# Performance work log

Measured on AMD Instinct MI355X. Metric: run time of the kernel, lower is better.

Reference implementation:

```python
import jax, jax.numpy as jnp
import numpy as np

B, H, O, M = 8192, 1024, 1024, 4

def setup_inputs() -> dict:
    key = jax.random.key(0)
    ks = jax.random.split(key, 8)
    state = jax.random.normal(ks[0], (B, H), dtype=jnp.float32)
    spectral_entropy = jax.random.uniform(ks[1], (B, 1), dtype=jnp.float32)
    curvature = jax.random.normal(ks[2], (B, 1), dtype=jnp.float32)
    # learned params
    modulation_basis = jax.random.normal(ks[3], (M, H, O), dtype=jnp.float32)
    gate_w = jax.random.normal(ks[4], (1, M), dtype=jnp.float32) / jnp.sqrt(1.0)
    gate_b = jax.random.normal(ks[5], (M,), dtype=jnp.float32) * 0.01
    prj_w = jax.random.normal(ks[6], (H, O), dtype=jnp.float32) / jnp.sqrt(H)
    prj_b = jax.random.normal(ks[7], (O,), dtype=jnp.float32) * 0.01
    return {"state": state, "spectral_entropy": spectral_entropy, "curvature": curvature,
            "modulation_basis": modulation_basis, "gate_w": gate_w, "gate_b": gate_b,
            "prj_w": prj_w, "prj_b": prj_b}

def reference(state, spectral_entropy, curvature, modulation_basis, gate_w, gate_b, prj_w, prj_b):
    # softmax gate over modes: [B, M]
    mod_weights = jax.nn.softmax(spectral_entropy @ gate_w + gate_b, axis=-1)
    # Algebraically fused form of einsum('bm,mho->bho') then einsum('bh,bho->bo'):
    # compute per-mode matvec results [B, M, O] (small), then mode-weighted sum.
    mode_out = jnp.einsum('bh,mho->bmo', state, modulation_basis)
    mischief_output = jnp.einsum('bm,bmo->bo', mod_weights, mode_out)
    base_output = state @ prj_w + prj_b
    mix = jax.nn.sigmoid(curvature)  # [B, 1]
    return (1.0 - mix) * base_output + mix * mischief_output
```

## Files before the change

### kernel.cpp

```cpp
#include <hip/hip_runtime.h>
#include <stdint.h>

typedef __attribute__((ext_vector_type(4))) float  float4v;
typedef __attribute__((ext_vector_type(8))) __bf16 bf16x8;
typedef __attribute__((ext_vector_type(8))) unsigned short ushort8;

#define B_DIM 8192
#define H_DIM 1024
#define O_DIM 1024

static __device__ __forceinline__ unsigned short f32_to_bf16(float f) {
  union { float f; unsigned int u; } v; v.f = f;
  unsigned int u = v.u;
  unsigned int r = u + 0x7FFFu + ((u >> 16) & 1u);
  return (unsigned short)(r >> 16);
}

__global__ void prep_coeff(const float* __restrict__ se, const float* __restrict__ curv,
                           const float* __restrict__ gw, const float* __restrict__ gb,
                           float* __restrict__ cfg) {
  int b = blockIdx.x * blockDim.x + threadIdx.x;
  if (b >= B_DIM) return;
  float s = se[b];
  float l0 = s * gw[0] + gb[0];
  float l1 = s * gw[1] + gb[1];
  float l2 = s * gw[2] + gb[2];
  float l3 = s * gw[3] + gb[3];
  float mx = fmaxf(fmaxf(l0, l1), fmaxf(l2, l3));
  float e0 = __expf(l0 - mx), e1 = __expf(l1 - mx), e2 = __expf(l2 - mx), e3 = __expf(l3 - mx);
  float mix = 1.0f / (1.0f + __expf(-curv[b]));
  float inv = mix / (e0 + e1 + e2 + e3);
  cfg[0 * B_DIM + b] = e0 * inv;
  cfg[1 * B_DIM + b] = e1 * inv;
  cfg[2 * B_DIM + b] = e2 * inv;
  cfg[3 * B_DIM + b] = e3 * inv;
  cfg[4 * B_DIM + b] = 1.0f - mix;
}

__global__ void cast_state(const float* __restrict__ src, unsigned short* __restrict__ dst, int n8) {
  int i = blockIdx.x * blockDim.x + threadIdx.x;
  if (i >= n8) return;
  float4v v0 = ((const float4v*)src)[i * 2];
  float4v v1 = ((const float4v*)src)[i * 2 + 1];
  ushort8 o;
  o[0] = f32_to_bf16(v0.x); o[1] = f32_to_bf16(v0.y);
  o[2] = f32_to_bf16(v0.z); o[3] = f32_to_bf16(v0.w);
  o[4] = f32_to_bf16(v1.x); o[5] = f32_to_bf16(v1.y);
  o[6] = f32_to_bf16(v1.z); o[7] = f32_to_bf16(v1.w);
  ((ushort8*)dst)[i] = o;
}

__global__ void transpose_cast(const float* __restrict__ basis, const float* __restrict__ prjw,
                               unsigned short* __restrict__ Wt) {
  __shared__ __align__(16) unsigned short t[64 * 72];
  int m = blockIdx.z;
  const float* src = (m < 4) ? (basis + (size_t)m * H_DIM * O_DIM) : prjw;
  int o0 = blockIdx.x * 64, h0 = blockIdx.y * 64;
  int tid = threadIdx.x;
  int r  = tid >> 4;
  int c4 = (tid & 15) * 4;
#pragma unroll
  for (int p = 0; p < 4; ++p) {
    int h = r + p * 16;
    float4v v = *(const float4v*)(src + (size_t)(h0 + h) * O_DIM + o0 + c4);
    t[(c4 + 0) * 72 + h] = f32_to_bf16(v.x);
    t[(c4 + 1) * 72 + h] = f32_to_bf16(v.y);
    t[(c4 + 2) * 72 + h] = f32_to_bf16(v.z);
    t[(c4 + 3) * 72 + h] = f32_to_bf16(v.w);
  }
  __syncthreads();
#pragma unroll
  for (int i = 0; i < 2; ++i) {
    int C = i * 256 + tid;
    int o = C >> 3, cc = C & 7;
    ushort8 val = *(const ushort8*)(t + o * 72 + cc * 8);
    *(ushort8*)(Wt + ((size_t)m * O_DIM + o0 + o) * H_DIM + h0 + cc * 8) = val;
  }
}

__global__ __launch_bounds__(256, 2)
void gemm_fused(const unsigned short* __restrict__ A,
                const unsigned short* __restrict__ Wt,
                const float* __restrict__ cfg,
                const float* __restrict__ prjb,
                float* __restrict__ out) {
  __shared__ __align__(16) unsigned char smem[59904];
  unsigned short* sA  = (unsigned short*)smem;
  unsigned short* sB  = (unsigned short*)(smem + 16384);
  float*          scf = (float*)(smem + 57344);

  const int tid  = threadIdx.x;
  const int lane = tid & 63;
  const int wave = tid >> 6;
  const int row0 = blockIdx.x * 128;
  const int col0 = blockIdx.y * 64;
  const int wrow = (wave >> 1) * 64;
  const int wcol = (wave & 1) * 32;
  const int q  = lane >> 4;
  const int ln = lane & 15;

  for (int i = tid; i < 5 * 128; i += 256)
    scf[i] = cfg[(i >> 7) * B_DIM + row0 + (i & 127)];

  int arow[4], acol[4];
#pragma unroll
  for (int j = 0; j < 4; ++j) {
    int L = (wave * 4 + j) * 64 + lane;
    arow[j] = L >> 3;
    acol[j] = (L & 7) ^ (arow[j] & 7);
  }
  int brow[2], bcol[2];
#pragma unroll
  for (int j = 0; j < 2; ++j) {
    int L = (wave * 2 + j) * 64 + lane;
    brow[j] = L >> 3;
    bcol[j] = (L & 7) ^ (brow[j] & 7);
  }

  float4v acc[5][4][2];
#pragma unroll
  for (int m = 0; m < 5; ++m)
#pragma unroll
    for (int i = 0; i < 4; ++i)
#pragma unroll
      for (int j = 0; j < 2; ++j)
        acc[m][i][j] = (float4v){0.f, 0.f, 0.f, 0.f};

  for (int kt = 0; kt < 16; ++kt) {
    const int k0 = kt * 64;
    __syncthreads();
#pragma unroll
    for (int j = 0; j < 4; ++j) {
      const unsigned short* ga = A + (size_t)(row0 + arow[j]) * H_DIM + k0 + acol[j] * 8;
      unsigned short* la = sA + (wave * 4 + j) * 512;
      __builtin_amdgcn_global_load_lds(
          (const __attribute__((address_space(1))) void*)ga,
          (__attribute__((address_space(3))) void*)la, 16, 0, 0);
    }
#pragma unroll
    for (int m = 0; m < 5; ++m) {
      const unsigned short* Wm = Wt + (size_t)m * O_DIM * H_DIM;
#pragma unroll
      for (int j = 0; j < 2; ++j) {
        const unsigned short* gw = Wm + (size_t)(col0 + brow[j]) * H_DIM + k0 + bcol[j] * 8;
        unsigned short* lb = sB + m * 4096 + (wave * 2 + j) * 512;
        __builtin_amdgcn_global_load_lds(
            (const __attribute__((address_space(1))) void*)gw,
            (__attribute__((address_space(3))) void*)lb, 16, 0, 0);
      }
    }
    __syncthreads();

#pragma unroll
    for (int kk = 0; kk < 2; ++kk) {
      bf16x8 af[4];
#pragma unroll
      for (int t = 0; t < 4; ++t) {
        int ra = wrow + t * 16 + ln;
        int ca = (kk * 4 + q) ^ (ra & 7);
        af[t] = *(const bf16x8*)(sA + ra * 64 + ca * 8);
      }
#pragma unroll
      for (int m = 0; m < 5; ++m) {
        bf16x8 b0, b1;
        {
          int rb = wcol + ln;
          int cb = (kk * 4 + q) ^ (rb & 7);
          b0 = *(const bf16x8*)(sB + m * 4096 + rb * 64 + cb * 8);
          int rb1 = wcol + 16 + ln;
          int cb1 = (kk * 4 + q) ^ (rb1 & 7);
          b1 = *(const bf16x8*)(sB + m * 4096 + rb1 * 64 + cb1 * 8);
        }
#pragma unroll
        for (int ti = 0; ti < 4; ++ti) {
          acc[m][ti][0] = __builtin_amdgcn_mfma_f32_16x16x32_bf16(af[ti], b0, acc[m][ti][0], 0, 0, 0);
          acc[m][ti][1] = __builtin_amdgcn_mfma_f32_16x16x32_bf16(af[ti], b1, acc[m][ti][1], 0, 0, 0);
        }
      }
    }
  }

  __syncthreads();
  float* fbuf = (float*)smem;
#pragma unroll
  for (int ti = 0; ti < 4; ++ti) {
    int rl = wrow + ti * 16 + q * 4;
#pragma unroll
    for (int tj = 0; tj < 2; ++tj) {
      int cc = wcol + tj * 16 + ln;
#pragma unroll
      for (int r = 0; r < 4; ++r) {
        float v = 0.f;
#pragma unroll
        for (int m = 0; m < 5; ++m)
          v += scf[m * 128 + rl + r] * acc[m][ti][tj][r];
        fbuf[(rl + r) * 68 + cc] = v;
      }
    }
  }
  __syncthreads();
#pragma unroll
  for (int i = 0; i < 8; ++i) {
    int L = i * 256 + tid;
    int row = L >> 4, c4 = L & 15;
    float4v v = *(const float4v*)(fbuf + row * 68 + c4 * 4);
    float cb = scf[4 * 128 + row];
    float4v pb = *(const float4v*)(prjb + col0 + c4 * 4);
    v += cb * pb;
    *(float4v*)(out + (size_t)(row0 + row) * O_DIM + col0 + c4 * 4) = v;
  }
}

extern "C" void kernel_launch(void* const* d_in, const int* in_sizes, int n_in,
                              void* d_out, int out_size, void* d_ws, size_t ws_size,
                              hipStream_t stream) {
  const float* state = (const float*)d_in[0];
  const float* se    = (const float*)d_in[1];
  const float* curv  = (const float*)d_in[2];
  const float* basis = (const float*)d_in[3];
  const float* gw    = (const float*)d_in[4];
  const float* gb    = (const float*)d_in[5];
  const float* prjw  = (const float*)d_in[6];
  const float* prjb  = (const float*)d_in[7];
  float* out = (float*)d_out;

  char* ws = (char*)d_ws;
  unsigned short* Abf = (unsigned short*)ws;
  unsigned short* Wt  = (unsigned short*)(ws + (size_t)16 * 1024 * 1024);
  float* cfg          = (float*)(ws + (size_t)28 * 1024 * 1024);

  prep_coeff<<<B_DIM / 256, 256, 0, stream>>>(se, curv, gw, gb, cfg);
  cast_state<<<(B_DIM * H_DIM / 8) / 256, 256, 0, stream>>>(state, Abf, B_DIM * H_DIM / 8);
  dim3 tg(O_DIM / 64, H_DIM / 64, 5);
  transpose_cast<<<tg, 256, 0, stream>>>(basis, prjw, Wt);
  dim3 gg(B_DIM / 128, O_DIM / 64);
  gemm_fused<<<gg, 256, 0, stream>>>(Abf, Wt, cfg, prjb, out);
}
```

Before: 184.0 us.

## Double-buffer GEMM K-loop with smaller K tile and merge prep kernels

The main GEMM now uses a two-stage LDS double buffer with a K tile of 32 instead of a single-buffered K tile of 64. The next stage's global-to-LDS loads are issued before computing the current stage, and there is one barrier per stage. The gate/softmax coefficients are computed inside the GEMM rather than in a separate kernel, and the state cast and weight transpose-cast are merged into one launch. The goal is to overlap memory loads with MFMA work and cut launch count, at the cost of a new swizzle scheme, more loop iterations and a shallower K tile per barrier.

```diff
diff --git a/kernel.cpp b/kernel.cpp
--- a/kernel.cpp
+++ b/kernel.cpp
@@ -16,78 +16,59 @@
   return (unsigned short)(r >> 16);
 }
 
-__global__ void prep_coeff(const float* __restrict__ se, const float* __restrict__ curv,
-                           const float* __restrict__ gw, const float* __restrict__ gb,
-                           float* __restrict__ cfg) {
-  int b = blockIdx.x * blockDim.x + threadIdx.x;
-  if (b >= B_DIM) return;
-  float s = se[b];
-  float l0 = s * gw[0] + gb[0];
-  float l1 = s * gw[1] + gb[1];
-  float l2 = s * gw[2] + gb[2];
-  float l3 = s * gw[3] + gb[3];
-  float mx = fmaxf(fmaxf(l0, l1), fmaxf(l2, l3));
-  float e0 = __expf(l0 - mx), e1 = __expf(l1 - mx), e2 = __expf(l2 - mx), e3 = __expf(l3 - mx);
-  float mix = 1.0f / (1.0f + __expf(-curv[b]));
-  float inv = mix / (e0 + e1 + e2 + e3);
-  cfg[0 * B_DIM + b] = e0 * inv;
-  cfg[1 * B_DIM + b] = e1 * inv;
-  cfg[2 * B_DIM + b] = e2 * inv;
-  cfg[3 * B_DIM + b] = e3 * inv;
-  cfg[4 * B_DIM + b] = 1.0f - mix;
-}
-
-__global__ void cast_state(const float* __restrict__ src, unsigned short* __restrict__ dst, int n8) {
-  int i = blockIdx.x * blockDim.x + threadIdx.x;
-  if (i >= n8) return;
-  float4v v0 = ((const float4v*)src)[i * 2];
-  float4v v1 = ((const float4v*)src)[i * 2 + 1];
-  ushort8 o;
-  o[0] = f32_to_bf16(v0.x); o[1] = f32_to_bf16(v0.y);
-  o[2] = f32_to_bf16(v0.z); o[3] = f32_to_bf16(v0.w);
-  o[4] = f32_to_bf16(v1.x); o[5] = f32_to_bf16(v1.y);
-  o[6] = f32_to_bf16(v1.z); o[7] = f32_to_bf16(v1.w);
-  ((ushort8*)dst)[i] = o;
-}
-
-__global__ void transpose_cast(const float* __restrict__ basis, const float* __restrict__ prjw,
-                               unsigned short* __restrict__ Wt) {
+__global__ void prep_inputs(const float* __restrict__ state,
+                            const float* __restrict__ basis,
+                            const float* __restrict__ prjw,
+                            unsigned short* __restrict__ Abf,
+                            unsigned short* __restrict__ Wt) {
   __shared__ __align__(16) unsigned short t[64 * 72];
-  int m = blockIdx.z;
-  const float* src = (m < 4) ? (basis + (size_t)m * H_DIM * O_DIM) : prjw;
-  int o0 = blockIdx.x * 64, h0 = blockIdx.y * 64;
+  int bb = blockIdx.x;
   int tid = threadIdx.x;
-  int r  = tid >> 4;
-  int c4 = (tid & 15) * 4;
-#pragma unroll
-  for (int p = 0; p < 4; ++p) {
-    int h = r + p * 16;
-    float4v v = *(const float4v*)(src + (size_t)(h0 + h) * O_DIM + o0 + c4);
-    t[(c4 + 0) * 72 + h] = f32_to_bf16(v.x);
-    t[(c4 + 1) * 72 + h] = f32_to_bf16(v.y);
-    t[(c4 + 2) * 72 + h] = f32_to_bf16(v.z);
-    t[(c4 + 3) * 72 + h] = f32_to_bf16(v.w);
-  }
-  __syncthreads();
-#pragma unroll
-  for (int i = 0; i < 2; ++i) {
-    int C = i * 256 + tid;
-    int o = C >> 3, cc = C & 7;
-    ushort8 val = *(const ushort8*)(t + o * 72 + cc * 8);
-    *(ushort8*)(Wt + ((size_t)m * O_DIM + o0 + o) * H_DIM + h0 + cc * 8) = val;
+  if (bb < 1280) {
+    int m = bb >> 8, panel = bb & 255;
+    int o0 = (panel & 15) * 64, h0 = (panel >> 4) * 64;
+    const float* src = (m < 4) ? (basis + (size_t)m * H_DIM * O_DIM) : prjw;
+    int r  = tid >> 4;
+    int c4 = (tid & 15) * 4;
+#pragma unroll
+    for (int p = 0; p < 4; ++p) {
+      int h = r + p * 16;
+      float4v v = *(const float4v*)(src + (size_t)(h0 + h) * O_DIM + o0 + c4);
+      t[(c4 + 0) * 72 + h] = f32_to_bf16(v.x);
+      t[(c4 + 1) * 72 + h] = f32_to_bf16(v.y);
+      t[(c4 + 2) * 72 + h] = f32_to_bf16(v.z);
+      t[(c4 + 3) * 72 + h] = f32_to_bf16(v.w);
+    }
+    __syncthreads();
+#pragma unroll
+    for (int i = 0; i < 2; ++i) {
+      int C = i * 256 + tid;
+      int o = C >> 3, cc = C & 7;
+      ushort8 val = *(const ushort8*)(t + o * 72 + cc * 8);
+      *(ushort8*)(Wt + ((size_t)m * O_DIM + o0 + o) * H_DIM + h0 + cc * 8) = val;
+    }
+  } else {
+    int i = (bb - 1280) * 256 + tid;
+    float4v v0 = ((const float4v*)state)[i * 2];
+    float4v v1 = ((const float4v*)state)[i * 2 + 1];
+    ushort8 o;
+    o[0] = f32_to_bf16(v0.x); o[1] = f32_to_bf16(v0.y);
+    o[2] = f32_to_bf16(v0.z); o[3] = f32_to_bf16(v0.w);
+    o[4] = f32_to_bf16(v1.x); o[5] = f32_to_bf16(v1.y);
+    o[6] = f32_to_bf16(v1.z); o[7] = f32_to_bf16(v1.w);
+    ((ushort8*)Abf)[i] = o;
   }
 }
 
 __global__ __launch_bounds__(256, 2)
 void gemm_fused(const unsigned short* __restrict__ A,
                 const unsigned short* __restrict__ Wt,
-                const float* __restrict__ cfg,
+                const float* __restrict__ se, const float* __restrict__ curv,
+                const float* __restrict__ gw, const float* __restrict__ gb,
                 const float* __restrict__ prjb,
                 float* __restrict__ out) {
   __shared__ __align__(16) unsigned char smem[59904];
-  unsigned short* sA  = (unsigned short*)smem;
-  unsigned short* sB  = (unsigned short*)(smem + 16384);
-  float*          scf = (float*)(smem + 57344);
+  float* scf = (float*)(smem + 57344);
 
   const int tid  = threadIdx.x;
   const int lane = tid & 63;
@@ -99,22 +80,44 @@
   const int q  = lane >> 4;
   const int ln = lane & 15;
 
-  for (int i = tid; i < 5 * 128; i += 256)
-    scf[i] = cfg[(i >> 7) * B_DIM + row0 + (i & 127)];
-
-  int arow[4], acol[4];
-#pragma unroll
-  for (int j = 0; j < 4; ++j) {
-    int L = (wave * 4 + j) * 64 + lane;
-    arow[j] = L >> 3;
-    acol[j] = (L & 7) ^ (arow[j] & 7);
-  }
-  int brow[2], bcol[2];
+  if (tid < 128) {
+    int b = row0 + tid;
+    float s = se[b];
+    float l0 = fmaf(s, gw[0], gb[0]);
+    float l1 = fmaf(s, gw[1], gb[1]);
+    float l2 = fmaf(s, gw[2], gb[2]);
+    float l3 = fmaf(s, gw[3], gb[3]);
+    float mx = fmaxf(fmaxf(l0, l1), fmaxf(l2, l3));
+    float e0 = __expf(l0 - mx), e1 = __expf(l1 - mx);
+    float e2 = __expf(l2 - mx), e3 = __expf(l3 - mx);
+    float mix = 1.0f / (1.0f + __expf(-curv[b]));
+    float inv = mix / (e0 + e1 + e2 + e3);
+    scf[0 * 128 + tid] = e0 * inv;
+    scf[1 * 128 + tid] = e1 * inv;
+    scf[2 * 128 + tid] = e2 * inv;
+    scf[3 * 128 + tid] = e3 * inv;
+    scf[4 * 128 + tid] = 1.0f - mix;
+  }
+
+  const unsigned short* gA[2];
+  unsigned int ldsA[2];
 #pragma unroll
   for (int j = 0; j < 2; ++j) {
-    int L = (wave * 2 + j) * 64 + lane;
-    brow[j] = L >> 3;
-    bcol[j] = (L & 7) ^ (brow[j] & 7);
+    int C = (wave * 2 + j) * 64 + lane;
+    int row = C >> 2, pos = C & 3;
+    int g = pos ^ ((row >> 1) & 3);
+    gA[j] = A + (size_t)(row0 + row) * H_DIM + g * 8;
+    ldsA[j] = (wave * 2 + j) * 1024;
+  }
+  const unsigned short* gB[5];
+  unsigned int ldsBbase = 8192 + wave * 1024;
+  {
+    int C = wave * 64 + lane;
+    int row = C >> 2, pos = C & 3;
+    int g = pos ^ ((row >> 1) & 3);
+#pragma unroll
+    for (int m = 0; m < 5; ++m)
+      gB[m] = Wt + (size_t)m * O_DIM * H_DIM + (size_t)(col0 + row) * H_DIM + g * 8;
   }
 
   float4v acc[5][4][2];
@@ -126,59 +129,65 @@
       for (int j = 0; j < 2; ++j)
         acc[m][i][j] = (float4v){0.f, 0.f, 0.f, 0.f};
 
-  for (int kt = 0; kt < 16; ++kt) {
-    const int k0 = kt * 64;
+#define ISSUE_STAGE(s)                                                          \
+  do {                                                                          \
+    const int _buf = (s) & 1;                                                   \
+    const int _k = (s) * 32;                                                    \
+    unsigned char* _base = smem + _buf * 28672;                                 \
+    _Pragma("unroll")                                                           \
+    for (int _j = 0; _j < 2; ++_j)                                              \
+      __builtin_amdgcn_global_load_lds(                                         \
+          (const __attribute__((address_space(1))) void*)(gA[_j] + _k),         \
+          (__attribute__((address_space(3))) void*)(_base + ldsA[_j]), 16, 0, 0);\
+    _Pragma("unroll")                                                           \
+    for (int _m = 0; _m < 5; ++_m)                                              \
+      __builtin_amdgcn_global_load_lds(                                         \
+          (const __attribute__((address_space(1))) void*)(gB[_m] + _k),         \
+          (__attribute__((address_space(3))) void*)(_base + ldsBbase + _m * 4096),\
+          16, 0, 0);                                                            \
+  } while (0)
+
+#define COMPUTE_STAGE(s)                                                        \
+  do {                                                                          \
+    const unsigned short* _sA = (const unsigned short*)(smem + ((s) & 1) * 28672);\
+    const unsigned short* _sB = _sA + 4096;                                     \
+    bf16x8 _af[4];                                                              \
+    _Pragma("unroll")                                                           \
+    for (int _t = 0; _t < 4; ++_t) {                                            \
+      int _ra = wrow + _t * 16 + ln;                                            \
+      int _ps = q ^ ((_ra >> 1) & 3);                                           \
+      _af[_t] = *(const bf16x8*)(_sA + _ra * 32 + _ps * 8);                     \
+    }                                                                           \
+    _Pragma("unroll")                                                           \
+    for (int _m = 0; _m < 5; ++_m) {                                            \
+      bf16x8 _b0, _b1;                                                          \
+      {                                                                         \
+        int _rb = wcol + ln;                                                    \
+        int _p0 = q ^ ((_rb >> 1) & 3);                                         \
+        _b0 = *(const bf16x8*)(_sB + _m * 2048 + _rb * 32 + _p0 * 8);           \
+        int _r1 = wcol + 16 + ln;                                               \
+        int _p1 = q ^ ((_r1 >> 1) & 3);                                         \
+        _b1 = *(const bf16x8*)(_sB + _m * 2048 + _r1 * 32 + _p1 * 8);           \
+      }                                                                         \
+      _Pragma("unroll")                                                         \
+      for (int _ti = 0; _ti < 4; ++_ti) {                                       \
+        acc[_m][_ti][0] = __builtin_amdgcn_mfma_f32_16x16x32_bf16(              \
+            _af[_ti], _b0, acc[_m][_ti][0], 0, 0, 0);                           \
+        acc[_m][_ti][1] = __builtin_amdgcn_mfma_f32_16x16x32_bf16(              \
+            _af[_ti], _b1, acc[_m][_ti][1], 0, 0, 0);                           \
+      }                                                                         \
+    }                                                                           \
+  } while (0)
+
+  ISSUE_STAGE(0);
+  __syncthreads();
+#pragma unroll 2
+  for (int s = 0; s < 31; ++s) {
+    ISSUE_STAGE(s + 1);
+    COMPUTE_STAGE(s);
     __syncthreads();
-#pragma unroll
-    for (int j = 0; j < 4; ++j) {
-      const unsigned short* ga = A + (size_t)(row0 + arow[j]) * H_DIM + k0 + acol[j] * 8;
-      unsigned short* la = sA + (wave * 4 + j) * 512;
-      __builtin_amdgcn_global_load_lds(
-          (const __attribute__((address_space(1))) void*)ga,
-          (__attribute__((address_space(3))) void*)la, 16, 0, 0);
-    }
-#pragma unroll
-    for (int m = 0; m < 5; ++m) {
-      const unsigned short* Wm = Wt + (size_t)m * O_DIM * H_DIM;
-#pragma unroll
-      for (int j = 0; j < 2; ++j) {
-        const unsigned short* gw = Wm + (size_t)(col0 + brow[j]) * H_DIM + k0 + bcol[j] * 8;
-        unsigned short* lb = sB + m * 4096 + (wave * 2 + j) * 512;
-        __builtin_amdgcn_global_load_lds(
-            (const __attribute__((address_space(1))) void*)gw,
-            (__attribute__((address_space(3))) void*)lb, 16, 0, 0);
-      }
-    }
-    __syncthreads();
-
-#pragma unroll
-    for (int kk = 0; kk < 2; ++kk) {
-      bf16x8 af[4];
-#pragma unroll
-      for (int t = 0; t < 4; ++t) {
-        int ra = wrow + t * 16 + ln;
-        int ca = (kk * 4 + q) ^ (ra & 7);
-        af[t] = *(const bf16x8*)(sA + ra * 64 + ca * 8);
-      }
-#pragma unroll
-      for (int m = 0; m < 5; ++m) {
-        bf16x8 b0, b1;
-        {
-          int rb = wcol + ln;
-          int cb = (kk * 4 + q) ^ (rb & 7);
-          b0 = *(const bf16x8*)(sB + m * 4096 + rb * 64 + cb * 8);
-          int rb1 = wcol + 16 + ln;
-          int cb1 = (kk * 4 + q) ^ (rb1 & 7);
-          b1 = *(const bf16x8*)(sB + m * 4096 + rb1 * 64 + cb1 * 8);
-        }
-#pragma unroll
-        for (int ti = 0; ti < 4; ++ti) {
-          acc[m][ti][0] = __builtin_amdgcn_mfma_f32_16x16x32_bf16(af[ti], b0, acc[m][ti][0], 0, 0, 0);
-          acc[m][ti][1] = __builtin_amdgcn_mfma_f32_16x16x32_bf16(af[ti], b1, acc[m][ti][1], 0, 0, 0);
-        }
-      }
-    }
-  }
+  }
+  COMPUTE_STAGE(31);
 
   __syncthreads();
   float* fbuf = (float*)smem;
@@ -209,6 +218,8 @@
     v += cb * pb;
     *(float4v*)(out + (size_t)(row0 + row) * O_DIM + col0 + c4 * 4) = v;
   }
+#undef ISSUE_STAGE
+#undef COMPUTE_STAGE
 }
 
 extern "C" void kernel_launch(void* const* d_in, const int* in_sizes, int n_in,
@@ -227,12 +238,8 @@
   char* ws = (char*)d_ws;
   unsigned short* Abf = (unsigned short*)ws;
   unsigned short* Wt  = (unsigned short*)(ws + (size_t)16 * 1024 * 1024);
-  float* cfg          = (float*)(ws + (size_t)28 * 1024 * 1024);
-
-  prep_coeff<<<B_DIM / 256, 256, 0, stream>>>(se, curv, gw, gb, cfg);
-  cast_state<<<(B_DIM * H_DIM / 8) / 256, 256, 0, stream>>>(state, Abf, B_DIM * H_DIM / 8);
-  dim3 tg(O_DIM / 64, H_DIM / 64, 5);
-  transpose_cast<<<tg, 256, 0, stream>>>(basis, prjw, Wt);
+
+  prep_inputs<<<5376, 256, 0, stream>>>(state, basis, prjw, Abf, Wt);
   dim3 gg(B_DIM / 128, O_DIM / 64);
-  gemm_fused<<<gg, 256, 0, stream>>>(Abf, Wt, cfg, prjb, out);
-}
+  gemm_fused<<<gg, 256, 0, stream>>>(Abf, Wt, se, curv, gw, gb, prjb, out);
+}
```

Measured after the change: 183.7 us. About the same (-0.1%).
